# Optimization experiments

Hardware: AMD Instinct MI355X
Metric: run time of the kernel (lower is better)

Reference implementation:

```python
import jax, jax.numpy as jnp
import numpy as np

PH, PW = 7, 7          # pooled output size (fixed by offset shape in module)
SPP = 2                # sample_per_part: bilinear samples per bin edge
SS = 0.0625            # spatial_scale = 1/16
TRANS_STD = 0.1


def setup_inputs() -> dict:
    key = jax.random.key(0)
    k1, k2, k3, k4, k5 = jax.random.split(key, 5)
    B, C, H, W = 8, 256, 168, 168
    N = 512
    img = W / SS  # input-image extent = 2688
    features = jax.random.normal(k1, (B, C, H, W), dtype=jnp.float32)
    bidx = jax.random.randint(k2, (N,), 0, B).astype(jnp.float32)
    xs = jnp.sort(jax.random.uniform(k3, (N, 2), minval=0.0, maxval=img - 1.0), axis=1)
    ys = jnp.sort(jax.random.uniform(k4, (N, 2), minval=0.0, maxval=img - 1.0), axis=1)
    rois = jnp.stack([bidx, xs[:, 0], ys[:, 0],
                      jnp.minimum(xs[:, 1] + 16.0, img - 1.0),
                      jnp.minimum(ys[:, 1] + 16.0, img - 1.0)], axis=1)
    offset = jax.random.normal(k5, (N, 2, PH, PW), dtype=jnp.float32)
    return {"features": features, "rois": rois, "offset": offset}


def _deform_roi_pool(features, rois, offset):
    B, C, H, W = features.shape
    off = offset * TRANS_STD  # module scales offsets by trans_std
    bidx = jax.lax.stop_gradient(rois[:, 0]).astype(jnp.int32)
    x1, y1, x2, y2 = rois[:, 1], rois[:, 2], rois[:, 3], rois[:, 4]
    # DCN kernel ROI geometry (0.5-pixel aligned, min size 0.1)
    sw = x1 * SS - 0.5
    sh = y1 * SS - 0.5
    rw = jnp.maximum((x2 + 1.0) * SS - 0.5 - sw, 0.1)
    rh = jnp.maximum((y2 + 1.0) * SS - 0.5 - sh, 0.1)
    bin_w, bin_h = rw / PW, rh / PH
    sub_w, sub_h = bin_w / SPP, bin_h / SPP

    e5 = lambda v: v[:, None, None, None, None]  # [N] -> [N,1,1,1,1]
    pw = jnp.arange(PW, dtype=features.dtype).reshape(1, 1, PW, 1, 1)
    ph = jnp.arange(PH, dtype=features.dtype).reshape(1, PH, 1, 1, 1)
    iw = (jnp.arange(SPP, dtype=features.dtype) + 0.5).reshape(1, 1, 1, 1, SPP)
    ih = (jnp.arange(SPP, dtype=features.dtype) + 0.5).reshape(1, 1, 1, SPP, 1)
    offx = off[:, 0][:, :, :, None, None]  # [N,PH,PW,1,1]
    offy = off[:, 1][:, :, :, None, None]

    # sample coords [N,PH,PW,SPP,SPP]: bin start + per-bin learned shift + sub-sample
    x = e5(sw) + pw * e5(bin_w) + offx * e5(rw) + iw * e5(sub_w)
    y = e5(sh) + ph * e5(bin_h) + offy * e5(rh) + ih * e5(sub_h)

    valid = (x > -0.5) & (x < W - 0.5) & (y > -0.5) & (y < H - 0.5)
    xc = jnp.clip(x, 0.0, W - 1.0)
    yc = jnp.clip(y, 0.0, H - 1.0)
    x0f, y0f = jnp.floor(xc), jnp.floor(yc)
    lx, ly = xc - x0f, yc - y0f
    x0 = x0f.astype(jnp.int32)
    y0 = y0f.astype(jnp.int32)
    x1i = jnp.minimum(x0 + 1, W - 1)
    y1i = jnp.minimum(y0 + 1, H - 1)

    # flat gather over (batch, h, w), channels vectorized
    featf = jnp.transpose(features, (0, 2, 3, 1)).reshape(B * H * W, C)
    base = e5(bidx) * (H * W)
    g = lambda yy, xx: featf[base + yy * W + xx]  # [N,PH,PW,SPP,SPP,C]

    w00 = ((1 - ly) * (1 - lx))[..., None]
    w01 = ((1 - ly) * lx)[..., None]
    w10 = (ly * (1 - lx))[..., None]
    w11 = (ly * lx)[..., None]
    val = w00 * g(y0, x0) + w01 * g(y0, x1i) + w10 * g(y1i, x0) + w11 * g(y1i, x1i)
    val = jnp.where(valid[..., None], val, 0.0)

    s = val.sum(axis=(3, 4))                                   # [N,PH,PW,C]
    cnt = valid.sum(axis=(3, 4)).astype(features.dtype)[..., None]
    out = jnp.where(cnt > 0, s / jnp.maximum(cnt, 1.0), 0.0)
    return jnp.transpose(out, (0, 3, 1, 2))                    # [N,C,PH,PW]


def reference(features, rois, offset):
    return _deform_roi_pool(features, rois, offset)
```

## Files before the change

### kernel.cpp

```cpp
#include <hip/hip_runtime.h>
#include <hip/hip_fp16.h>


#define PH_ 7
#define PW_ 7
#define SPP_ 2
#define SS_ 0.0625f
#define TRANS_STD_ 0.1f
#define B_ 8
#define C_ 256
#define H_ 168
#define W_ 168
#define N_ 512
#define HW_ (H_ * W_)
#define HW4_ (HW_ / 4)
#define BINS_ (PH_ * PW_)
#define NSUB_ (SPP_ * SPP_)
#define BLK_ 1024
#define PLN_ (HW_ + W_ + 4)
#define CPB_ 8
#define NPROD_ 512
#define CRPC_ 10

#define WS_LIST_OFF_   B_
#define WS_DESCA_OFF_I (B_ + B_ * N_)
#define DESCA_INTS_    (N_ * BINS_ * 4)
#define WS_DESCW_OFF_I (WS_DESCA_OFF_I + DESCA_INTS_)
#define DESCW_FLOATS_  (N_ * BINS_ * NSUB_ * 4)
#define WS_NEEDED_     ((size_t)(WS_DESCW_OFF_I + DESCW_FLOATS_) * 4)

__global__ __launch_bounds__(64) void build_all(
    const float* __restrict__ rois,
    const float* __restrict__ offset,
    int* __restrict__ ws)
{
    const int blk = blockIdx.x;
    const int t   = threadIdx.x;

    if (blk == N_) {
        if (t < B_) ws[t] = 0;
        __syncthreads();
        for (int r = t; r < N_; r += 64) {
            const int b = (int)rois[r * 5 + 0];
            const int pos = atomicAdd(&ws[b], 1);
            ws[WS_LIST_OFF_ + b * N_ + pos] = r;
        }
        return;
    }

    const int r   = blk;
    const int bin = t;
    if (bin >= BINS_) return;
    const int ph = bin / PW_;
    const int pw = bin - ph * PW_;

    const float x1r = rois[r * 5 + 1];
    const float y1r = rois[r * 5 + 2];
    const float x2r = rois[r * 5 + 3];
    const float y2r = rois[r * 5 + 4];

    const float sw    = x1r * SS_ - 0.5f;
    const float sh    = y1r * SS_ - 0.5f;
    const float rw    = fmaxf((x2r + 1.0f) * SS_ - 0.5f - sw, 0.1f);
    const float rh    = fmaxf((y2r + 1.0f) * SS_ - 0.5f - sh, 0.1f);
    const float bin_w = rw * (1.0f / PW_);
    const float bin_h = rh * (1.0f / PH_);
    const float sub_w = bin_w * (1.0f / SPP_);
    const float sub_h = bin_h * (1.0f / SPP_);

    const float offx = offset[((r * 2 + 0) * PH_ + ph) * PW_ + pw] * TRANS_STD_;
    const float offy = offset[((r * 2 + 1) * PH_ + ph) * PW_ + pw] * TRANS_STD_;

    const float bx = sw + (float)pw * bin_w + offx * rw;
    const float by = sh + (float)ph * bin_h + offy * rh;

    unsigned idx[NSUB_];
    float w00[NSUB_], w01[NSUB_], w10[NSUB_], w11[NSUB_];
    int   vals[NSUB_];
    int   cnt = 0;
#pragma unroll
    for (int s = 0; s < NSUB_; ++s) {
        const int ihs = s >> 1;
        const int iws = s & 1;
        const float x = bx + ((float)iws + 0.5f) * sub_w;
        const float y = by + ((float)ihs + 0.5f) * sub_h;
        const int valid = (x > -0.5f) && (x < (float)W_ - 0.5f) &&
                          (y > -0.5f) && (y < (float)H_ - 0.5f);
        const float xc = fminf(fmaxf(x, 0.0f), (float)(W_ - 1));
        const float yc = fminf(fmaxf(y, 0.0f), (float)(H_ - 1));
        const float x0f = floorf(xc);
        const float y0f = floorf(yc);
        const int x0 = (int)x0f;
        const int y0 = (int)y0f;
        const float lx = xc - x0f;
        const float ly = yc - y0f;
        idx[s] = (unsigned)(y0 * W_ + x0);
        w00[s] = (1.0f - ly) * (1.0f - lx);
        w01[s] = (1.0f - ly) * lx;
        w10[s] = ly * (1.0f - lx);
        w11[s] = ly * lx;
        vals[s] = valid;
        cnt += valid;
    }
    const float inv = (cnt > 0) ? (1.0f / (float)cnt) : 0.0f;

    uint4*  descA = reinterpret_cast<uint4*> (ws + WS_DESCA_OFF_I);
    float4* descW = reinterpret_cast<float4*>(ws + WS_DESCW_OFF_I);

    const int rb = r * BINS_ + bin;
#pragma unroll
    for (int s = 0; s < NSUB_; ++s) {
        const float f = vals[s] ? inv : 0.0f;
        float4 w;
        w.x = w00[s] * f;
        w.y = w01[s] * f;
        w.z = w10[s] * f;
        w.w = w11[s] * f;
        descW[(size_t)rb * NSUB_ + s] = w;
    }
    uint4 a4;
    a4.x = idx[0]; a4.y = idx[1]; a4.z = idx[2]; a4.w = idx[3];
    descA[rb] = a4;
}

__global__ __launch_bounds__(BLK_, 4) void droi_pool_pc(
    const float* __restrict__ features,
    float* __restrict__ out,
    const int* __restrict__ ws)
{
    __shared__ __half bufs[2][PLN_];

    const int c0  = blockIdx.x * CPB_;
    const int b   = blockIdx.y;
    const int tid = threadIdx.x;

    const float4* __restrict__ fbase =
        reinterpret_cast<const float4*>(features + (size_t)b * C_ * HW_);

    for (int i = HW_ + tid; i < PLN_; i += BLK_) {
        bufs[0][i] = __float2half(0.0f);
        bufs[1][i] = __float2half(0.0f);
    }
    {
        const float4* __restrict__ f4 = fbase + (size_t)c0 * HW4_;
        for (int i = tid; i < HW4_; i += BLK_) {
            const float4 v = f4[i];
            union { __half2 h[2]; float2 f2; } u;
            u.h[0].x = __float2half(v.x); u.h[0].y = __float2half(v.y);
            u.h[1].x = __float2half(v.z); u.h[1].y = __float2half(v.w);
            *reinterpret_cast<float2*>(&bufs[0][i * 4]) = u.f2;
        }
    }
    __syncthreads();

    const int cnt_b = ws[b];
    const int* __restrict__ list = ws + WS_LIST_OFF_ + b * N_;
    const uint4* __restrict__ descA =
        reinterpret_cast<const uint4*>(ws + WS_DESCA_OFF_I);
    const float4* __restrict__ descW =
        reinterpret_cast<const float4*>(ws + WS_DESCW_OFF_I);

    const bool consumer = (tid >= NPROD_);
    const int  t   = tid - NPROD_;
    const int  q   = consumer ? (t / BINS_) : 0;
    const int  bin = consumer ? (t - q * BINS_) : 0;
    const bool lane_ok = consumer && (q < CRPC_);

    for (int p = 0; p < CPB_; ++p) {
        const int c = c0 + p;
        const __half* __restrict__ cur = bufs[p & 1];
        __half*       __restrict__ nxt = bufs[(p & 1) ^ 1];

        if (!consumer) {
            if (p + 1 < CPB_) {
                const float4* __restrict__ f4 = fbase + (size_t)(c + 1) * HW4_;
                for (int i = tid; i < HW4_; i += NPROD_) {
                    const float4 v = f4[i];
                    union { __half2 h[2]; float2 f2; } u;
                    u.h[0].x = __float2half(v.x); u.h[0].y = __float2half(v.y);
                    u.h[1].x = __float2half(v.z); u.h[1].y = __float2half(v.w);
                    *reinterpret_cast<float2*>(&nxt[i * 4]) = u.f2;
                }
            }
        } else {
            for (int base = 0; base < cnt_b; base += CRPC_) {
                const int idx = base + q;
                if (lane_ok && (idx < cnt_b)) {
                    const int r  = list[idx];
                    const int rb = r * BINS_ + bin;

                    const uint4 a4 = descA[rb];
                    const float4* __restrict__ wp = descW + (size_t)rb * NSUB_;

                    float acc = 0.0f;
#pragma unroll
                    for (int s = 0; s < NSUB_; ++s) {
                        const float4 w = wp[s];
                        const int a = (int)((&a4.x)[s]);
                        const float f00 = __half2float(cur[a]);
                        const float f01 = __half2float(cur[a + 1]);
                        const float f10 = __half2float(cur[a + W_]);
                        const float f11 = __half2float(cur[a + W_ + 1]);
                        acc += w.x * f00 + w.y * f01 + w.z * f10 + w.w * f11;
                    }
                    out[((size_t)r * C_ + c) * BINS_ + bin] = acc;
                }
            }
        }

        __syncthreads();
    }
}

__global__ __launch_bounds__(64) void droi_pool_fallback(
    const float* __restrict__ features,
    const float* __restrict__ rois,
    const float* __restrict__ offset,
    float* __restrict__ out)
{
    const int blk  = blockIdx.x;
    const int n    = blk >> 8;
    const int c    = blk & 255;
    const int lane = threadIdx.x;
    if (lane >= BINS_) return;
    const int ph = lane / PW_;
    const int pw = lane % PW_;

    const float r0  = rois[n * 5 + 0];
    const float x1r = rois[n * 5 + 1];
    const float y1r = rois[n * 5 + 2];
    const float x2r = rois[n * 5 + 3];
    const float y2r = rois[n * 5 + 4];
    const int   b   = (int)r0;

    const float sw    = x1r * SS_ - 0.5f;
    const float sh    = y1r * SS_ - 0.5f;
    const float rw    = fmaxf((x2r + 1.0f) * SS_ - 0.5f - sw, 0.1f);
    const float rh    = fmaxf((y2r + 1.0f) * SS_ - 0.5f - sh, 0.1f);
    const float bin_w = rw / PW_;
    const float bin_h = rh / PH_;
    const float sub_w = bin_w / SPP_;
    const float sub_h = bin_h / SPP_;

    const float offx = offset[((n * 2 + 0) * PH_ + ph) * PW_ + pw] * TRANS_STD_;
    const float offy = offset[((n * 2 + 1) * PH_ + ph) * PW_ + pw] * TRANS_STD_;

    const float bx = sw + (float)pw * bin_w + offx * rw;
    const float by = sh + (float)ph * bin_h + offy * rh;

    const float* __restrict__ f =
        features + (size_t)(b * C_ + c) * (size_t)HW_;

    float s = 0.0f;
    int cnt = 0;
#pragma unroll
    for (int ihs = 0; ihs < SPP_; ++ihs) {
#pragma unroll
        for (int iws = 0; iws < SPP_; ++iws) {
            const float x = bx + ((float)iws + 0.5f) * sub_w;
            const float y = by + ((float)ihs + 0.5f) * sub_h;
            const bool valid = (x > -0.5f) && (x < (float)W_ - 0.5f) &&
                               (y > -0.5f) && (y < (float)H_ - 0.5f);
            const float xc = fminf(fmaxf(x, 0.0f), (float)(W_ - 1));
            const float yc = fminf(fmaxf(y, 0.0f), (float)(H_ - 1));
            const float x0f = floorf(xc);
            const float y0f = floorf(yc);
            const float lx = xc - x0f;
            const float ly = yc - y0f;
            const int x0 = (int)x0f;
            const int y0 = (int)y0f;
            const int x1i = min(x0 + 1, W_ - 1);
            const int y1i = min(y0 + 1, H_ - 1);
            const float f00 = f[y0  * W_ + x0 ];
            const float f01 = f[y0  * W_ + x1i];
            const float f10 = f[y1i * W_ + x0 ];
            const float f11 = f[y1i * W_ + x1i];
            const float v = (1.0f - ly) * (1.0f - lx) * f00 +
                            (1.0f - ly) * lx          * f01 +
                            ly          * (1.0f - lx) * f10 +
                            ly          * lx          * f11;
            if (valid) { s += v; cnt += 1; }
        }
    }
    const float res = (cnt > 0) ? (s / (float)cnt) : 0.0f;
    out[(size_t)(n * C_ + c) * BINS_ + lane] = res;
}

extern "C" void kernel_launch(void* const* d_in, const int* in_sizes, int n_in,
                              void* d_out, int out_size, void* d_ws, size_t ws_size,
                              hipStream_t stream) {
    const float* features = (const float*)d_in[0];
    const float* rois     = (const float*)d_in[1];
    const float* offset   = (const float*)d_in[2];
    float*       out      = (float*)d_out;

    if (ws_size >= WS_NEEDED_) {
        int* ws = (int*)d_ws;
        hipLaunchKernelGGL(build_all, dim3(N_ + 1), dim3(64), 0, stream,
                           rois, offset, ws);
        hipLaunchKernelGGL(droi_pool_pc, dim3(C_ / CPB_, B_), dim3(BLK_),
                           0, stream, features, out, ws);
    } else {
        hipLaunchKernelGGL(droi_pool_fallback, dim3(N_ * C_), dim3(64), 0, stream,
                           features, rois, offset, out);
    }
}
```

Measured before the change: 381.6 us.

## Replace fp16 producer/consumer double buffer with direct global-to-LDS fp32 plane loads

Drops the split between producer and consumer threads and the fp16 double-buffered planes. Each channel plane is now loaded straight into a single fp32 shared buffer with the global_load_lds builtin, which bypasses registers and removes the conversion step. After a barrier, all 1024 threads compute bins, 20 ROIs per round instead of 10. The cost is that loading and compute no longer overlap across channels, and the result is more precise because the plane stays in fp32.

Measured after the change: 356.0 us. 1.07x faster.

```diff
diff --git a/kernel.cpp b/kernel.cpp
--- a/kernel.cpp
+++ b/kernel.cpp
@@ -17,10 +17,11 @@
 #define BINS_ (PH_ * PW_)
 #define NSUB_ (SPP_ * SPP_)
 #define BLK_ 1024
+#define RPC_ 20
 #define PLN_ (HW_ + W_ + 4)
 #define CPB_ 8
-#define NPROD_ 512
-#define CRPC_ 10
+#define FULL_ROUNDS_ 6
+#define TAIL_THREADS_ (HW4_ - FULL_ROUNDS_ * BLK_)
 
 #define WS_LIST_OFF_   B_
 #define WS_DESCA_OFF_I (B_ + B_ * N_)
@@ -28,6 +29,14 @@
 #define WS_DESCW_OFF_I (WS_DESCA_OFF_I + DESCA_INTS_)
 #define DESCW_FLOATS_  (N_ * BINS_ * NSUB_ * 4)
 #define WS_NEEDED_     ((size_t)(WS_DESCW_OFF_I + DESCW_FLOATS_) * 4)
+
+__device__ __forceinline__ void gload16(const void* g, void* l)
+{
+    __builtin_amdgcn_global_load_lds(
+        (const __attribute__((address_space(1))) unsigned int*)g,
+        (__attribute__((address_space(3))) unsigned int*)l,
+        16, 0, 0);
+}
 
 __global__ __launch_bounds__(64) void build_all(
     const float* __restrict__ rois,
@@ -123,12 +132,12 @@
     descA[rb] = a4;
 }
 
-__global__ __launch_bounds__(BLK_, 4) void droi_pool_pc(
+__global__ __launch_bounds__(BLK_, 4) void droi_pool_gl(
     const float* __restrict__ features,
     float* __restrict__ out,
     const int* __restrict__ ws)
 {
-    __shared__ __half bufs[2][PLN_];
+    __shared__ float plane[PLN_];
 
     const int c0  = blockIdx.x * CPB_;
     const int b   = blockIdx.y;
@@ -137,21 +146,7 @@
     const float4* __restrict__ fbase =
         reinterpret_cast<const float4*>(features + (size_t)b * C_ * HW_);
 
-    for (int i = HW_ + tid; i < PLN_; i += BLK_) {
-        bufs[0][i] = __float2half(0.0f);
-        bufs[1][i] = __float2half(0.0f);
-    }
-    {
-        const float4* __restrict__ f4 = fbase + (size_t)c0 * HW4_;
-        for (int i = tid; i < HW4_; i += BLK_) {
-            const float4 v = f4[i];
-            union { __half2 h[2]; float2 f2; } u;
-            u.h[0].x = __float2half(v.x); u.h[0].y = __float2half(v.y);
-            u.h[1].x = __float2half(v.z); u.h[1].y = __float2half(v.w);
-            *reinterpret_cast<float2*>(&bufs[0][i * 4]) = u.f2;
-        }
-    }
-    __syncthreads();
+    for (int i = HW_ + tid; i < PLN_; i += BLK_) plane[i] = 0.0f;
 
     const int cnt_b = ws[b];
     const int* __restrict__ list = ws + WS_LIST_OFF_ + b * N_;
@@ -160,51 +155,49 @@
     const float4* __restrict__ descW =
         reinterpret_cast<const float4*>(ws + WS_DESCW_OFF_I);
 
-    const bool consumer = (tid >= NPROD_);
-    const int  t   = tid - NPROD_;
-    const int  q   = consumer ? (t / BINS_) : 0;
-    const int  bin = consumer ? (t - q * BINS_) : 0;
-    const bool lane_ok = consumer && (q < CRPC_);
+    const int q   = tid / BINS_;
+    const int bin = tid - q * BINS_;
+    const bool lane_ok = (q < RPC_);
 
     for (int p = 0; p < CPB_; ++p) {
         const int c = c0 + p;
-        const __half* __restrict__ cur = bufs[p & 1];
-        __half*       __restrict__ nxt = bufs[(p & 1) ^ 1];
-
-        if (!consumer) {
-            if (p + 1 < CPB_) {
-                const float4* __restrict__ f4 = fbase + (size_t)(c + 1) * HW4_;
-                for (int i = tid; i < HW4_; i += NPROD_) {
-                    const float4 v = f4[i];
-                    union { __half2 h[2]; float2 f2; } u;
-                    u.h[0].x = __float2half(v.x); u.h[0].y = __float2half(v.y);
-                    u.h[1].x = __float2half(v.z); u.h[1].y = __float2half(v.w);
-                    *reinterpret_cast<float2*>(&nxt[i * 4]) = u.f2;
+
+        {
+            const float4* __restrict__ f4 = fbase + (size_t)c * HW4_;
+#pragma unroll
+            for (int i = 0; i < FULL_ROUNDS_; ++i) {
+                const int slot = tid + i * BLK_;
+                gload16(f4 + slot, &plane[slot * 4]);
+            }
+            if (tid < TAIL_THREADS_) {
+                const int slot = tid + FULL_ROUNDS_ * BLK_;
+                gload16(f4 + slot, &plane[slot * 4]);
+            }
+        }
+        __syncthreads();
+
+        for (int base = 0; base < cnt_b; base += RPC_) {
+            const int idx    = base + q;
+            const bool active = lane_ok && (idx < cnt_b);
+            if (active) {
+                const int r  = list[idx];
+                const int rb = r * BINS_ + bin;
+
+                const uint4 a4 = descA[rb];
+                const float4* __restrict__ wp = descW + (size_t)rb * NSUB_;
+
+                float acc = 0.0f;
+#pragma unroll
+                for (int s = 0; s < NSUB_; ++s) {
+                    const float4 w = wp[s];
+                    const int a = (int)((&a4.x)[s]);
+                    const float f00 = plane[a];
+                    const float f01 = plane[a + 1];
+                    const float f10 = plane[a + W_];
+                    const float f11 = plane[a + W_ + 1];
+                    acc += w.x * f00 + w.y * f01 + w.z * f10 + w.w * f11;
                 }
-            }
-        } else {
-            for (int base = 0; base < cnt_b; base += CRPC_) {
-                const int idx = base + q;
-                if (lane_ok && (idx < cnt_b)) {
-                    const int r  = list[idx];
-                    const int rb = r * BINS_ + bin;
-
-                    const uint4 a4 = descA[rb];
-                    const float4* __restrict__ wp = descW + (size_t)rb * NSUB_;
-
-                    float acc = 0.0f;
-#pragma unroll
-                    for (int s = 0; s < NSUB_; ++s) {
-                        const float4 w = wp[s];
-                        const int a = (int)((&a4.x)[s]);
-                        const float f00 = __half2float(cur[a]);
-                        const float f01 = __half2float(cur[a + 1]);
-                        const float f10 = __half2float(cur[a + W_]);
-                        const float f11 = __half2float(cur[a + W_ + 1]);
-                        acc += w.x * f00 + w.y * f01 + w.z * f10 + w.w * f11;
-                    }
-                    out[((size_t)r * C_ + c) * BINS_ + bin] = acc;
-                }
+                out[((size_t)r * C_ + c) * BINS_ + bin] = acc;
             }
         }
 
@@ -298,7 +291,7 @@
         int* ws = (int*)d_ws;
         hipLaunchKernelGGL(build_all, dim3(N_ + 1), dim3(64), 0, stream,
                            rois, offset, ws);
-        hipLaunchKernelGGL(droi_pool_pc, dim3(C_ / CPB_, B_), dim3(BLK_),
+        hipLaunchKernelGGL(droi_pool_gl, dim3(C_ / CPB_, B_), dim3(BLK_),
                            0, stream, features, out, ws);
     } else {
         hipLaunchKernelGGL(droi_pool_fallback, dim3(N_ * C_), dim3(64), 0, stream,
```
